# Optimization experiments

Measured on AMD Instinct MI355X. Metric: run time of the kernel, lower is better.

## Reference

```python
import jax, jax.numpy as jnp
import numpy as np

B, S = 4, 1024          # sequences, tokens per sequence (equal-length prefill)
T = B * S               # total ragged tokens
H, D = 16, 128          # heads, head_size
HID = H * D             # hidden_size = 2048
THETA = 10000.0


def setup_inputs() -> dict:
    key = jax.random.key(0)
    k0, k1, k2, k3 = jax.random.split(key, 4)
    hidden_states = jax.random.normal(k0, (T, HID), jnp.float32) * 0.02
    # real RoPE tables (PositionRotaryEmbedding.static), [T, D//2]
    inv_freq = 1.0 / (THETA ** (jnp.arange(0, D, 2, dtype=jnp.float32) / D))
    pos = jnp.tile(jnp.arange(S, dtype=jnp.float32), B)  # position resets per sequence
    ang = pos[:, None] * inv_freq[None, :]
    cos, sin = jnp.cos(ang), jnp.sin(ang)
    w_attn = jax.random.normal(k1, (3 * HID, HID), jnp.float32) * 0.02
    b_attn = jax.random.normal(k2, (3 * HID,), jnp.float32) * 0.02
    w_proj = jax.random.normal(k3, (HID, HID), jnp.float32) * 0.02
    cu_seqlens = (jnp.arange(B + 1, dtype=jnp.int32) * S)
    return {"hidden_states": hidden_states, "cos": cos, "sin": sin,
            "w_attn": w_attn, "b_attn": b_attn, "w_proj": w_proj,
            "cu_seqlens": cu_seqlens}


def _rope(x, cos, sin):
    # x: [T, H, D]; cos/sin: [T, D//2]; rotate-half (neox) style
    x1, x2 = jnp.split(x, 2, axis=-1)
    c, s = cos[:, None, :], sin[:, None, :]
    return jnp.concatenate([x1 * c - x2 * s, x2 * c + x1 * s], axis=-1)


def reference(hidden_states, cos, sin, w_attn, b_attn, w_proj, cu_seqlens):
    scale = D ** -0.5
    qkv = hidden_states @ w_attn.T + b_attn          # [T, 3*HID]
    q = qkv[:, :HID].reshape(T, H, D)
    k = qkv[:, HID:2 * HID].reshape(T, H, D)
    v = qkv[:, 2 * HID:].reshape(T, H, D)
    q = _rope(q, cos, sin)
    k = _rope(k, cos, sin)
    # equal-length ragged batch -> [B, S, H, D]; causal flash-attn (prefill path)
    qb = q.reshape(B, S, H, D)
    kb = k.reshape(B, S, H, D)
    vb = v.reshape(B, S, H, D)
    scores = jnp.einsum('bqhd,bkhd->bhqk', qb, kb) * scale
    causal = jnp.tril(jnp.ones((S, S), dtype=bool))
    scores = jnp.where(causal[None, None], scores, jnp.finfo(scores.dtype).min)
    p = jax.nn.softmax(scores, axis=-1)
    o = jnp.einsum('bhqk,bkhd->bqhd', p, vb).reshape(T, HID)
    return o @ w_proj.T                               # c_proj, no bias
```

## Files before the change

kernel.cpp:

```cpp
#include <hip/hip_runtime.h>

typedef __bf16 bf16x8 __attribute__((ext_vector_type(8)));
typedef __bf16 bf16x4 __attribute__((ext_vector_type(4)));
typedef float  f32x4  __attribute__((ext_vector_type(4)));

#define T_TOT 4096
#define SEQ   1024
#define BATCH 4
#define HEADS 16
#define DIM   128
#define HIDN  2048
#define QKVW  6144

__device__ __forceinline__ void gld_lds16(const void* g, void* l) {
  __builtin_amdgcn_global_load_lds(
      (const __attribute__((address_space(1))) unsigned int*)g,
      (__attribute__((address_space(3))) unsigned int*)l, 16, 0, 0);
}

__global__ void f2b_kernel(const float* __restrict__ in, __bf16* __restrict__ out, int n) {
  int i = (blockIdx.x * 256 + threadIdx.x) * 4;
  if (i >= n) return;
  const float4 v = *(const float4*)(in + i);
  bf16x4 o;
  o[0] = (__bf16)v.x; o[1] = (__bf16)v.y; o[2] = (__bf16)v.z; o[3] = (__bf16)v.w;
  *(bf16x4*)(out + i) = o;
}

template<int BIAS, typename OUT_T>
__global__ __launch_bounds__(512, 4) void gemm_pl(
    const __bf16* __restrict__ A, int lda,
    const __bf16* __restrict__ B, int ldb,
    const float* __restrict__ bias,
    OUT_T* __restrict__ C, int ldc, int K, int nby)
{
  __shared__ __bf16 sA[3 * 128 * 32];
  __shared__ __bf16 sB[3 * 256 * 32];
  const int tid = threadIdx.x;
  const int w = tid >> 6, lane = tid & 63;
  const int lq = lane & 15, lg = lane >> 4;
  const int wm = w >> 2, wn = w & 3;

  const int nwg = gridDim.x;
  const int cpx = nwg >> 3;
  const int bid = blockIdx.x;
  const int wgid = (bid & 7) * cpx + (bid >> 3);
  const int by = wgid % nby, bx = wgid / nby;
  const int bm = by * 128, bn = bx * 256;

  const int srow = tid >> 2;
  const int scol = ((tid & 3) ^ (srow & 3)) * 8;
  const __bf16* gA = A + (size_t)(bm + srow) * lda + scol;
  const __bf16* gB = B + (size_t)(bn + srow) * ldb + scol;
  const size_t strB = (size_t)128 * ldb;
  __bf16* dA = &sA[w * 512];
  __bf16* dB = &sB[w * 512];

  const int NT = K >> 5;

#define STAGE(t, bf) {                                              \
    gld_lds16(gA + (size_t)(t) * 32, dA + (bf) * 4096);             \
    const __bf16* sb_ = gB + (size_t)(t) * 32;                      \
    gld_lds16(sb_, dB + (bf) * 8192);                               \
    gld_lds16(sb_ + strB, dB + (bf) * 8192 + 4096); }

  f32x4 acc[4][4] = {};

  const int colo = (lg ^ (lq & 3)) * 8;
  const int offA = (wm * 64 + lq) * 32 + colo;
  const int offB = (wn * 64 + lq) * 32 + colo;

  STAGE(0, 0); STAGE(1, 1);
  asm volatile("s_waitcnt vmcnt(3)" ::: "memory");
  __builtin_amdgcn_s_barrier();

  bf16x8 a[4], b[4];
  {
    const __bf16* pA = &sA[offA];
    const __bf16* pB = &sB[offB];
#pragma unroll
    for (int m = 0; m < 4; ++m) a[m] = *(const bf16x8*)(pA + m * 512);
#pragma unroll
    for (int n = 0; n < 4; ++n) b[n] = *(const bf16x8*)(pB + n * 512);
  }

  int bcur = 0;
  for (int t = 0; t < NT; ++t) {
    int bstg = bcur + 2; if (bstg >= 3) bstg -= 3;
    const bool st = (t + 2) < NT;
    if (st) STAGE(t + 2, bstg);

    asm volatile("s_waitcnt lgkmcnt(0)" ::: "memory");
    __builtin_amdgcn_sched_barrier(0);
    __builtin_amdgcn_s_setprio(1);
#pragma unroll
    for (int m = 0; m < 4; ++m)
#pragma unroll
      for (int n = 0; n < 4; ++n)
        acc[m][n] = __builtin_amdgcn_mfma_f32_16x16x32_bf16(a[m], b[n], acc[m][n], 0, 0, 0);
    __builtin_amdgcn_s_setprio(0);

    if (t + 1 < NT) {
      if (st) { asm volatile("s_waitcnt vmcnt(3)" ::: "memory"); }
      else    { asm volatile("s_waitcnt vmcnt(0)" ::: "memory"); }
      const int bnext = (bcur + 1 == 3) ? 0 : bcur + 1;
      const __bf16* pA = &sA[bnext * 4096 + offA];
      const __bf16* pB = &sB[bnext * 8192 + offB];
#pragma unroll
      for (int m = 0; m < 4; ++m) a[m] = *(const bf16x8*)(pA + m * 512);
#pragma unroll
      for (int n = 0; n < 4; ++n) b[n] = *(const bf16x8*)(pB + n * 512);
    }
    __builtin_amdgcn_s_barrier();
    bcur = (bcur + 1 == 3) ? 0 : bcur + 1;
  }
#undef STAGE

#pragma unroll
  for (int n = 0; n < 4; ++n) {
    const int col = bn + wn * 64 + n * 16 + lq;
    const float bv = BIAS ? bias[col] : 0.0f;
#pragma unroll
    for (int m = 0; m < 4; ++m)
#pragma unroll
      for (int r = 0; r < 4; ++r) {
        const int row = bm + wm * 64 + m * 16 + lg * 4 + r;
        C[(size_t)row * ldc + col] = (OUT_T)(acc[m][n][r] + bv);
      }
  }
}

__global__ __launch_bounds__(256) void pack_kernel(const __bf16* __restrict__ qkv,
                                                   const float* __restrict__ cosb,
                                                   const float* __restrict__ sinb,
                                                   __bf16* __restrict__ Qp,
                                                   __bf16* __restrict__ Kp,
                                                   __bf16* __restrict__ Vt)
{
  __shared__ __bf16 tile[64][136];
  const int bh = blockIdx.y, b = bh >> 4, h = bh & 15;
  const int s0 = blockIdx.x * 64;
  const int tid = threadIdx.x;
  const int j0 = (tid & 7) * 8;
  const float qsc = 0.08838834764831845f;

#pragma unroll
  for (int it = 0; it < 2; ++it) {
    const int r = (tid >> 3) + it * 32;
    const int s = s0 + r;
    const size_t t = (size_t)b * SEQ + s;
    float cc[8], ss[8];
    *(float4*)&cc[0] = *(const float4*)&cosb[t * 64 + j0];
    *(float4*)&cc[4] = *(const float4*)&cosb[t * 64 + j0 + 4];
    *(float4*)&ss[0] = *(const float4*)&sinb[t * 64 + j0];
    *(float4*)&ss[4] = *(const float4*)&sinb[t * 64 + j0 + 4];
    const __bf16* src = qkv + t * QKVW + h * DIM;
    const bf16x8 q1 = *(const bf16x8*)(src + j0);
    const bf16x8 q2 = *(const bf16x8*)(src + 64 + j0);
    const bf16x8 k1 = *(const bf16x8*)(src + HIDN + j0);
    const bf16x8 k2 = *(const bf16x8*)(src + HIDN + 64 + j0);
    bf16x8 oq1, oq2, ok1, ok2;
#pragma unroll
    for (int jj = 0; jj < 8; ++jj) {
      const float c = cc[jj], sn = ss[jj];
      const float a1 = (float)q1[jj], a2 = (float)q2[jj];
      const float b1 = (float)k1[jj], b2 = (float)k2[jj];
      oq1[jj] = (__bf16)((a1 * c - a2 * sn) * qsc);
      oq2[jj] = (__bf16)((a2 * c + a1 * sn) * qsc);
      ok1[jj] = (__bf16)(b1 * c - b2 * sn);
      ok2[jj] = (__bf16)(b2 * c + b1 * sn);
    }
    __bf16* dq = Qp + ((size_t)bh * SEQ + s) * DIM + j0;
    __bf16* dk = Kp + ((size_t)bh * SEQ + s) * DIM + j0;
    *(bf16x8*)dq = oq1; *(bf16x8*)(dq + 64) = oq2;
    *(bf16x8*)dk = ok1; *(bf16x8*)(dk + 64) = ok2;
  }

#pragma unroll
  for (int i = 0; i < 4; ++i) {
    const int r = (tid >> 4) + i * 16;
    const int c = (tid & 15) * 8;
    *(bf16x8*)&tile[r][c] =
        *(const bf16x8*)&qkv[((size_t)b * SEQ + s0 + r) * QKVW + 2 * HIDN + h * DIM + c];
  }
  __syncthreads();
#pragma unroll
  for (int i = 0; i < 4; ++i) {
    const int d = (tid >> 3) + i * 32;
    const int scc = (tid & 7) * 8;
    bf16x8 v;
#pragma unroll
    for (int jj = 0; jj < 8; ++jj) v[jj] = tile[scc + jj][d];
    *(bf16x8*)&Vt[((size_t)bh * DIM + d) * SEQ + s0 + scc] = v;
  }
}

__global__ __launch_bounds__(256, 2) void attn_kernel(const __bf16* __restrict__ Qp,
                                                      const __bf16* __restrict__ Kp,
                                                      const __bf16* __restrict__ Vt,
                                                      __bf16* __restrict__ O)
{
  __shared__ __bf16 sK[2][64 * 128];
  __shared__ __bf16 sV[2][128 * 64];
  __shared__ __bf16 sP[4][32 * 64];
  const int w = threadIdx.x >> 6, lane = threadIdx.x & 63;
  const int lq = lane & 15, lg = lane >> 4;
  const int bh = blockIdx.y, b = bh >> 4, h = bh & 15;
  const int qb = ((int)blockIdx.x + bh) & 7;
  const int q0 = qb * 128 + w * 32;
  const int NTb = 2 * qb + 2;
  const int kend = q0 + 32;

  const __bf16* Qh = Qp + (size_t)bh * SEQ * DIM;
  const __bf16* Kh = Kp + (size_t)bh * SEQ * DIM;
  const __bf16* Vh = Vt + (size_t)bh * DIM * SEQ;

  const int krow = lane >> 4;
  const int kgr  = lane & 15;
  const int vrow = lane >> 3;
  const int vgr  = lane & 7;
  const __bf16* Vsrc = Vh + (size_t)(w * 32 + vrow) * SEQ + (vgr ^ vrow) * 8;

  auto ASTAGE = [&](int ktn, int p) {
#pragma unroll
    for (int i = 0; i < 4; ++i) {
      const int rb = w * 16 + i * 4;
      gld_lds16(Kh + (size_t)(ktn + rb + krow) * DIM + (kgr ^ (i * 4 + krow)) * 8,
                &sK[p][rb * DIM]);
    }
#pragma unroll
    for (int i = 0; i < 4; ++i) {
      gld_lds16(Vsrc + (size_t)i * 8 * SEQ + ktn, &sV[p][(w * 32 + i * 8) * 64]);
    }
  };

  bf16x8 aq[2][4];
#pragma unroll
  for (int m = 0; m < 2; ++m)
#pragma unroll
    for (int kk = 0; kk < 4; ++kk)
      aq[m][kk] = *(const bf16x8*)(Qh + (size_t)(q0 + m * 16 + lq) * DIM + kk * 32 + lg * 8);

  f32x4 accO[2][8] = {};
  float mrow[2][4], lrow[2][4];
#pragma unroll
  for (int m = 0; m < 2; ++m)
#pragma unroll
    for (int r = 0; r < 4; ++r) { mrow[m][r] = -1e30f; lrow[m][r] = 0.0f; }

  ASTAGE(0, 0);
  asm volatile("s_waitcnt vmcnt(0)" ::: "memory");
  __builtin_amdgcn_s_barrier();

  int p = 0;
  for (int t = 0; t < NTb; ++t) {
    const int kt = t * 64;
    if (t + 1 < NTb) ASTAGE(kt + 64, p ^ 1);

    if (kt < kend) {
      f32x4 s[2][4] = {};
#pragma unroll
      for (int n = 0; n < 4; ++n) {
        const int rowb = (n * 16 + lq) * DIM;
#pragma unroll
        for (int kk = 0; kk < 4; ++kk) {
          const bf16x8 bk = *(const bf16x8*)&sK[p][rowb + ((4 * kk + lg) ^ lq) * 8];
#pragma unroll
          for (int m = 0; m < 2; ++m)
            s[m][n] = __builtin_amdgcn_mfma_f32_16x16x32_bf16(aq[m][kk], bk, s[m][n], 0, 0, 0);
        }
      }
      if (kt + 63 > q0) {
#pragma unroll
        for (int n = 0; n < 4; ++n) {
          const int kpos = kt + n * 16 + lq;
#pragma unroll
          for (int m = 0; m < 2; ++m)
#pragma unroll
            for (int r = 0; r < 4; ++r)
              if (kpos > q0 + m * 16 + lg * 4 + r) s[m][n][r] = -1e30f;
        }
      }
#pragma unroll
      for (int m = 0; m < 2; ++m) {
#pragma unroll
        for (int r = 0; r < 4; ++r) {
          float mx = fmaxf(fmaxf(s[m][0][r], s[m][1][r]), fmaxf(s[m][2][r], s[m][3][r]));
          mx = fmaxf(mx, __shfl_xor(mx, 1));
          mx = fmaxf(mx, __shfl_xor(mx, 2));
          mx = fmaxf(mx, __shfl_xor(mx, 4));
          mx = fmaxf(mx, __shfl_xor(mx, 8));
          const float mnew = fmaxf(mrow[m][r], mx);
          const float alpha = __expf(mrow[m][r] - mnew);
          mrow[m][r] = mnew;
          float rs = 0.0f;
#pragma unroll
          for (int n = 0; n < 4; ++n) {
            const float pv = __expf(s[m][n][r] - mnew);
            s[m][n][r] = pv;
            rs += pv;
          }
          rs += __shfl_xor(rs, 1); rs += __shfl_xor(rs, 2);
          rs += __shfl_xor(rs, 4); rs += __shfl_xor(rs, 8);
          lrow[m][r] = lrow[m][r] * alpha + rs;
#pragma unroll
          for (int f = 0; f < 8; ++f) accO[m][f][r] *= alpha;
        }
      }
#pragma unroll
      for (int m = 0; m < 2; ++m)
#pragma unroll
        for (int n = 0; n < 4; ++n)
#pragma unroll
          for (int r = 0; r < 4; ++r) {
            const int prow = m * 16 + lg * 4 + r;
            const int cb = (n * 16 + lq) * 2;
            const int addr = prow * 128 + (((cb >> 4) ^ (prow & 7)) << 4) + (cb & 15);
            *(__bf16*)((char*)&sP[w][0] + addr) = (__bf16)s[m][n][r];
          }
      asm volatile("s_waitcnt lgkmcnt(0)" ::: "memory");
#pragma unroll
      for (int kk2 = 0; kk2 < 2; ++kk2) {
        bf16x8 ap[2];
#pragma unroll
        for (int m = 0; m < 2; ++m) {
          const int prow = m * 16 + lq;
          ap[m] = *(const bf16x8*)((char*)&sP[w][0] +
                   prow * 128 + (((4 * kk2 + lg) ^ (lq & 7)) << 4));
        }
#pragma unroll
        for (int f = 0; f < 8; ++f) {
          const bf16x8 bv = *(const bf16x8*)&sV[p][(f * 16 + lq) * 64 +
                                                   ((4 * kk2 + lg) ^ (lq & 7)) * 8];
#pragma unroll
          for (int m = 0; m < 2; ++m)
            accO[m][f] = __builtin_amdgcn_mfma_f32_16x16x32_bf16(ap[m], bv, accO[m][f], 0, 0, 0);
        }
      }
    }
    asm volatile("s_waitcnt vmcnt(0)" ::: "memory");
    __builtin_amdgcn_s_barrier();
    p ^= 1;
  }

#pragma unroll
  for (int m = 0; m < 2; ++m)
#pragma unroll
    for (int f = 0; f < 8; ++f)
#pragma unroll
      for (int r = 0; r < 4; ++r) {
        const float v = accO[m][f][r] / lrow[m][r];
        O[((size_t)b * SEQ + q0 + m * 16 + lg * 4 + r) * HIDN + h * DIM + f * 16 + lq] = (__bf16)v;
      }
}

extern "C" void kernel_launch(void* const* d_in, const int* in_sizes, int n_in,
                              void* d_out, int out_size, void* d_ws, size_t ws_size,
                              hipStream_t stream)
{
  const float* hidden = (const float*)d_in[0];
  const float* cosb   = (const float*)d_in[1];
  const float* sinb   = (const float*)d_in[2];
  const float* w_attn = (const float*)d_in[3];
  const float* b_attn = (const float*)d_in[4];
  const float* w_proj = (const float*)d_in[5];

  char* ws = (char*)d_ws;
  __bf16* hid_bf   = (__bf16*)(ws);
  __bf16* wattn_bf = (__bf16*)(ws + 16777216);
  __bf16* wproj_bf = (__bf16*)(ws + 41943040);
  __bf16* qkv      = (__bf16*)(ws + 50331648);
  __bf16* Qp       = (__bf16*)(ws);
  __bf16* Kp       = (__bf16*)(ws + 16777216);
  __bf16* Vt       = (__bf16*)(ws + 100663296);
  __bf16* Obuf     = (__bf16*)(ws + 117440512);
  float* out = (float*)d_out;

  f2b_kernel<<<8192, 256, 0, stream>>>(hidden, hid_bf, T_TOT * HIDN);
  f2b_kernel<<<12288, 256, 0, stream>>>(w_attn, wattn_bf, 3 * HIDN * HIDN);
  f2b_kernel<<<4096, 256, 0, stream>>>(w_proj, wproj_bf, HIDN * HIDN);

  gemm_pl<1, __bf16><<<768, 512, 0, stream>>>(
      hid_bf, HIDN, wattn_bf, HIDN, b_attn, qkv, QKVW, HIDN, 32);

  pack_kernel<<<dim3(16, 64), 256, 0, stream>>>(qkv, cosb, sinb, Qp, Kp, Vt);
  attn_kernel<<<dim3(8, 64), 256, 0, stream>>>(Qp, Kp, Vt, Obuf);

  gemm_pl<0, float><<<256, 512, 0, stream>>>(
      Obuf, HIDN, wproj_bf, HIDN, nullptr, out, HIDN, HIDN, 32);
}
```

Baseline: 282.4 us.

## Add 256x256 eight-phase pipelined GEMM for QKV projection

Adds a new GEMM kernel that uses 256x256 output tiles with BK=64 and double-buffered LDS, replacing the previous 128x256 triple-buffered kernel for the QKV projection. Global-to-LDS loads are spread across eight MFMA phases, with barriers and raised wave priority, so memory traffic overlaps compute. The larger tile improves operand reuse and halves the grid, at the cost of 128 KB LDS, more registers (two waves per SIMD), and fewer workgroups to fill the CUs.

```diff
diff --git a/kernel.cpp b/kernel.cpp
--- a/kernel.cpp
+++ b/kernel.cpp
@@ -25,6 +25,122 @@
   bf16x4 o;
   o[0] = (__bf16)v.x; o[1] = (__bf16)v.y; o[2] = (__bf16)v.z; o[3] = (__bf16)v.w;
   *(bf16x4*)(out + i) = o;
+}
+
+template<int BIAS, typename OUT_T>
+__global__ __launch_bounds__(512, 2) void gemm_8p(
+    const __bf16* __restrict__ A, int lda,
+    const __bf16* __restrict__ B, int ldb,
+    const float* __restrict__ bias,
+    OUT_T* __restrict__ C, int ldc, int K, int nby)
+{
+  __shared__ __bf16 sA[2 * 256 * 64];
+  __shared__ __bf16 sB[2 * 256 * 64];
+  const int tid = threadIdx.x;
+  const int w = tid >> 6, lane = tid & 63;
+  const int lq = lane & 15, lg = lane >> 4;
+  const int wm = w >> 2, wn = w & 3;
+
+  const int nwg = gridDim.x, cpx = nwg >> 3, bid = blockIdx.x;
+  const int wgid = (bid & 7) * cpx + (bid >> 3);
+  const int by = wgid % nby, bx = wgid / nby;
+  const int bm = by * 256, bn = bx * 256;
+
+  const int srow = tid >> 3;
+  const int sgr  = (tid & 7) ^ (srow & 7);
+  const __bf16* gA = A + (size_t)(bm + srow) * lda + sgr * 8;
+  const __bf16* gB = B + (size_t)(bn + srow) * ldb + sgr * 8;
+  const int woff = w * 512;
+  const int NT = K >> 6;
+
+#define STGA(tt, R) gld_lds16(gA + (size_t)(R) * lda + (size_t)(tt) * 64, \
+                              &sA[((tt) & 1) * 16384 + (R) * 64 + woff])
+#define STGB(tt, R) gld_lds16(gB + (size_t)(R) * ldb + (size_t)(tt) * 64, \
+                              &sB[((tt) & 1) * 16384 + (R) * 64 + woff])
+
+  f32x4 acc[8][4] = {};
+
+  int rowA[8], rowB[4], colk[2];
+#pragma unroll
+  for (int m = 0; m < 8; ++m) rowA[m] = (wm * 128 + m * 16 + lq) * 64;
+#pragma unroll
+  for (int n = 0; n < 4; ++n) rowB[n] = (wn * 64 + n * 16 + lq) * 64;
+  colk[0] = (lg ^ (lq & 7)) * 8;
+  colk[1] = ((4 + lg) ^ (lq & 7)) * 8;
+
+  STGA(0, 0); STGA(0, 128); STGA(0, 64); STGA(0, 192);
+  STGB(0, 0); STGB(0, 64); STGB(0, 128); STGB(0, 192);
+  STGA(1, 0); STGA(1, 128);
+  asm volatile("s_waitcnt vmcnt(0)" ::: "memory");
+  __builtin_amdgcn_s_barrier();
+
+  bf16x8 a[4], b[4];
+  const int NI = NT >> 1;
+  for (int j = 0; j < NI; ++j) {
+    const int t0 = 2 * j, t1 = 2 * j + 1;
+#pragma unroll
+    for (int half = 0; half < 2; ++half) {
+      const int tc = half ? t1 : t0;
+      const __bf16* pA = &sA[(tc & 1) * 16384];
+      const __bf16* pB = &sB[(tc & 1) * 16384];
+#pragma unroll
+      for (int q = 0; q < 4; ++q) {
+        const int ks = q >> 1, mh = q & 1;
+        if (mh == 0) {
+#pragma unroll
+          for (int mi = 0; mi < 4; ++mi) a[mi] = *(const bf16x8*)(pA + rowA[mi] + colk[ks]);
+#pragma unroll
+          for (int n = 0; n < 4; ++n)    b[n]  = *(const bf16x8*)(pB + rowB[n] + colk[ks]);
+        } else {
+#pragma unroll
+          for (int mi = 0; mi < 4; ++mi) a[mi] = *(const bf16x8*)(pA + rowA[4 + mi] + colk[ks]);
+        }
+        const int p = half * 4 + q;
+        bool staged = false;
+        switch (p) {
+          case 0: if (t1 < NT)     { STGB(t1, 0);       STGB(t1, 64);       } break;
+          case 1: if (t1 < NT)     { STGB(t1, 128);     STGB(t1, 192);     } break;
+          case 2: if (t1 < NT)     { STGA(t1, 64);      STGA(t1, 192);     } break;
+          case 3: if (t0 + 2 < NT) { STGA(t0 + 2, 0);   STGA(t0 + 2, 128); staged = true; } break;
+          case 4: if (t0 + 2 < NT) { STGB(t0 + 2, 0);   STGB(t0 + 2, 64);  } break;
+          case 5: if (t0 + 2 < NT) { STGB(t0 + 2, 128); STGB(t0 + 2, 192); } break;
+          case 6: if (t0 + 2 < NT) { STGA(t0 + 2, 64);  STGA(t0 + 2, 192); } break;
+          case 7: if (t1 + 2 < NT) { STGA(t1 + 2, 0);   STGA(t1 + 2, 128); staged = true; } break;
+        }
+        __builtin_amdgcn_s_barrier();
+        asm volatile("s_waitcnt lgkmcnt(0)" ::: "memory");
+        __builtin_amdgcn_sched_barrier(0);
+        __builtin_amdgcn_s_setprio(1);
+#pragma unroll
+        for (int mi = 0; mi < 4; ++mi)
+#pragma unroll
+          for (int n = 0; n < 4; ++n)
+            acc[mh * 4 + mi][n] = __builtin_amdgcn_mfma_f32_16x16x32_bf16(
+                a[mi], b[n], acc[mh * 4 + mi][n], 0, 0, 0);
+        __builtin_amdgcn_s_setprio(0);
+        if (q == 3) {
+          if (staged) { asm volatile("s_waitcnt vmcnt(2)" ::: "memory"); }
+          else        { asm volatile("s_waitcnt vmcnt(0)" ::: "memory"); }
+        }
+        __builtin_amdgcn_s_barrier();
+      }
+    }
+  }
+#undef STGA
+#undef STGB
+
+#pragma unroll
+  for (int n = 0; n < 4; ++n) {
+    const int col = bn + wn * 64 + n * 16 + lq;
+    const float bv = BIAS ? bias[col] : 0.0f;
+#pragma unroll
+    for (int m = 0; m < 8; ++m)
+#pragma unroll
+      for (int r = 0; r < 4; ++r) {
+        const int row = bm + wm * 128 + m * 16 + lg * 4 + r;
+        C[(size_t)row * ldc + col] = (OUT_T)(acc[m][n][r] + bv);
+      }
+  }
 }
 
 template<int BIAS, typename OUT_T>
@@ -380,8 +496,8 @@
   f2b_kernel<<<12288, 256, 0, stream>>>(w_attn, wattn_bf, 3 * HIDN * HIDN);
   f2b_kernel<<<4096, 256, 0, stream>>>(w_proj, wproj_bf, HIDN * HIDN);
 
-  gemm_pl<1, __bf16><<<768, 512, 0, stream>>>(
-      hid_bf, HIDN, wattn_bf, HIDN, b_attn, qkv, QKVW, HIDN, 32);
+  gemm_8p<1, __bf16><<<384, 512, 0, stream>>>(
+      hid_bf, HIDN, wattn_bf, HIDN, b_attn, qkv, QKVW, HIDN, 16);
 
   pack_kernel<<<dim3(16, 64), 256, 0, stream>>>(qkv, cosb, sinb, Qp, Kp, Vt);
   attn_kernel<<<dim3(8, 64), 256, 0, stream>>>(Qp, Kp, Vt, Obuf);
```

After: 307.3 us. 1.09x slower.
